# Kernel optimization log

Measured on AMD Instinct MI355X. Metric: run time of the kernel, lower is better.

The kernel has to match this reference:

```python
import jax, jax.numpy as jnp
import numpy as np

B, C, H, W = 4, 128, 64, 64
HEADS, DH, MEM = 4, 32, 16
HID = HEADS * DH  # 128


def setup_inputs() -> dict:
    key = jax.random.key(0)
    k1, k2, k3, k4, k5 = jax.random.split(key, 5)
    return {
        "x": jax.random.normal(k1, (B, C, H, W), jnp.float32),
        "memory": jax.random.normal(k2, (1, C, 1, MEM), jnp.float32),
        "w_qkv": jax.random.normal(k3, (3 * HID, C), jnp.float32) * 0.05,  # conv1x1, bias=False
        "w_out": jax.random.normal(k4, (C, HID), jnp.float32) * 0.05,      # conv1x1 weight
        "b_out": jax.random.normal(k5, (C,), jnp.float32) * 0.01,          # conv1x1 bias
    }


def reference(x, memory, w_qkv, w_out, b_out):
    b, c, h, w = x.shape
    hw = h * w
    scale = DH ** -0.5

    # flatten spatial, append memory tokens along token axis
    x_flat = x.reshape(b, c, hw)                         # (b, c, hw)
    mem = jnp.broadcast_to(memory[:, :, 0, :], (b, c, MEM))
    x_ext = jnp.concatenate([x_flat, mem], axis=2)       # (b, c, n) n = hw + MEM

    # 1x1 conv QKV projection == channel matmul
    qkv = jnp.einsum('oc,bcn->bon', w_qkv, x_ext)        # (b, 3*HID, n)
    q, k, v = jnp.split(qkv, 3, axis=1)                  # each (b, HID, n)

    def to_heads(t):
        return t.reshape(b, HEADS, DH, -1)               # (b, h, d, n)

    q = to_heads(q) * scale
    k = to_heads(k)
    v = to_heads(v)

    sim = jnp.einsum('bhdi,bhdj->bhij', q, k)            # (b, h, n, n)
    attn = jax.nn.softmax(sim, axis=-1)                  # stable softmax (amax-sub inside)
    out = jnp.einsum('bhij,bhdj->bhid', attn, v)         # (b, h, n, d)

    out = out[:, :, :hw]                                 # drop memory-token queries
    out = out.transpose(0, 1, 3, 2).reshape(b, HID, h, w)  # b (h d) x y

    return jnp.einsum('oc,bchw->bohw', w_out, out) + b_out[None, :, None, None]
```

## Files before the change

kernel.cpp:

```cpp
#include <hip/hip_runtime.h>
#include <hip/hip_bf16.h>

constexpr int NQ   = 4096;
constexpr int NKV  = 4112;
constexpr int NP   = 4160;
constexpr int CDIM = 128;
constexpr int NSL  = 4;
constexpr float QSC = 0.17677669529663687f * 1.4426950408889634f;

typedef __attribute__((ext_vector_type(8)))  short bf16x8;
typedef __attribute__((ext_vector_type(4)))  short bf16x4;
typedef __attribute__((ext_vector_type(4)))  unsigned short u16x4;
typedef __attribute__((ext_vector_type(4)))  float f32x4;
typedef __attribute__((ext_vector_type(16))) float f32x16;

static __device__ __forceinline__ unsigned short bfbits(float f) {
  __hip_bfloat16 h = __float2bfloat16(f);
  return *reinterpret_cast<unsigned short*>(&h);
}
static __device__ __forceinline__ unsigned pk2(float a, float b) {
  return (unsigned)bfbits(a) | ((unsigned)bfbits(b) << 16);
}
static __device__ __forceinline__ float b2f(unsigned short u) {
  unsigned x = (unsigned)u << 16;
  return *reinterpret_cast<float*>(&x);
}

__global__ __launch_bounds__(256) void k1_qkv(
    const float* __restrict__ x, const float* __restrict__ memry,
    const float* __restrict__ wqkv, const float* __restrict__ wout,
    __hip_bfloat16* __restrict__ Qt, __hip_bfloat16* __restrict__ Kt,
    __hip_bfloat16* __restrict__ Vt, __hip_bfloat16* __restrict__ Wb) {
  __shared__ __align__(16) __hip_bfloat16 xt[64][136];
  const int b  = blockIdx.y;
  const int zz = blockIdx.z;
  const int nb = blockIdx.x * 64;
  const int t  = threadIdx.x;
  const int wv = t >> 6, ln = t & 63;

  if (blockIdx.x == 0 && b == 0 && zz == 0) {
    for (int i = t; i < CDIM * CDIM; i += 256) Wb[i] = __float2bfloat16(wout[i]);
  }

  {
    const int n = nb + ln;
    #pragma unroll
    for (int i = 0; i < 16; ++i) {
      const int c = wv * 32 + 2 * i;
      float v0 = 0.f, v1 = 0.f;
      if (n < NQ)        { v0 = x[((size_t)b * CDIM + c) * NQ + n];
                           v1 = x[((size_t)b * CDIM + c + 1) * NQ + n]; }
      else if (n < NKV)  { v0 = memry[c * 16 + (n - NQ)];
                           v1 = memry[(c + 1) * 16 + (n - NQ)]; }
      *reinterpret_cast<unsigned*>(&xt[ln][c]) =
          (unsigned)bfbits(v0) | ((unsigned)bfbits(v1) << 16);
    }
  }
  __syncthreads();

  const int li = ln & 15, g = ln >> 4;
  bf16x8 xa[4][4];
  #pragma unroll
  for (int nt = 0; nt < 4; ++nt)
    #pragma unroll
    for (int k = 0; k < 4; ++k)
      xa[nt][k] = *reinterpret_cast<const bf16x8*>(&xt[nt * 16 + li][k * 32 + 8 * g]);

  #pragma unroll
  for (int oi = 0; oi < 3; ++oi) {
    const int ot = zz * 12 + wv * 3 + oi;
    bf16x8 wf[4];
    #pragma unroll
    for (int k = 0; k < 4; ++k) {
      const float* wp = &wqkv[(size_t)(ot * 16 + li) * CDIM + k * 32 + 8 * g];
      const float4 f0 = *reinterpret_cast<const float4*>(wp);
      const float4 f1 = *reinterpret_cast<const float4*>(wp + 4);
      bf16x8 wc;
      wc[0] = (short)bfbits(f0.x); wc[1] = (short)bfbits(f0.y);
      wc[2] = (short)bfbits(f0.z); wc[3] = (short)bfbits(f0.w);
      wc[4] = (short)bfbits(f1.x); wc[5] = (short)bfbits(f1.y);
      wc[6] = (short)bfbits(f1.z); wc[7] = (short)bfbits(f1.w);
      wf[k] = wc;
    }
    #pragma unroll
    for (int nt = 0; nt < 4; ++nt) {
      f32x4 a; a[0] = a[1] = a[2] = a[3] = 0.f;
      if (ot < 16) {
        #pragma unroll
        for (int k = 0; k < 4; ++k)
          a = __builtin_amdgcn_mfma_f32_16x16x32_bf16(xa[nt][k], wf[k], a, 0, 0, 0);
        const int o = ot * 16 + li;
        const int h = (o >> 5) & 3, d = o & 31;
        if (ot < 8) {
          #pragma unroll
          for (int r = 0; r < 4; ++r) {
            const int n = nb + nt * 16 + 4 * g + r;
            Qt[((size_t)(b * 4 + h) * NP + n) * 32 + d] = __float2bfloat16(a[r] * QSC);
          }
        } else {
          #pragma unroll
          for (int r = 0; r < 4; ++r) {
            const int n = nb + nt * 16 + 4 * g + r;
            Kt[((size_t)(b * 4 + h) * NP + n) * 32 + d] = __float2bfloat16(a[r]);
          }
        }
      } else {
        #pragma unroll
        for (int k = 0; k < 4; ++k)
          a = __builtin_amdgcn_mfma_f32_16x16x32_bf16(wf[k], xa[nt][k], a, 0, 0, 0);
        #pragma unroll
        for (int r = 0; r < 4; ++r) {
          const int o = ot * 16 + 4 * g + r;
          const int h = (o >> 5) & 3, d = o & 31;
          const int n = nb + nt * 16 + li;
          Vt[((size_t)(b * 4 + h) * 32 + d) * NP + n] = __float2bfloat16(a[r]);
        }
      }
    }
  }
}


#if __has_builtin(__builtin_amdgcn_mfma_f32_32x32x8bf16_1k)
#define HAS_PV8 1
#else
#define HAS_PV8 0
#endif

#if HAS_PV8
__device__ __forceinline__ void half32(
    const bf16x8& kf0, const bf16x8& kf1,
    const bf16x4& vf0, const bf16x4& vf1, const bf16x4& vf2, const bf16x4& vf3,
    const bf16x8& q0, const bf16x8& q1, const f32x16& z,
    f32x16& acc, float& l0, float& l1, float& l2, float& l3) {
  __builtin_amdgcn_s_setprio(1);
  f32x16 s = __builtin_amdgcn_mfma_f32_32x32x16_bf16(kf0, q0, z, 0, 0, 0);
  s = __builtin_amdgcn_mfma_f32_32x32x16_bf16(kf1, q1, s, 0, 0, 0);
  __builtin_amdgcn_s_setprio(0);
  float p[16];
  #pragma unroll
  for (int r = 0; r < 16; ++r) p[r] = __builtin_amdgcn_exp2f(s[r]);
  l0 += (p[0] + p[1]) + (p[2] + p[3]);
  l1 += (p[4] + p[5]) + (p[6] + p[7]);
  l2 += (p[8] + p[9]) + (p[10] + p[11]);
  l3 += (p[12] + p[13]) + (p[14] + p[15]);
  union UU { unsigned u[2]; bf16x4 v; };
  UU a0, a1, a2, a3;
  a0.u[0] = pk2(p[0], p[1]);   a0.u[1] = pk2(p[2], p[3]);
  a1.u[0] = pk2(p[4], p[5]);   a1.u[1] = pk2(p[6], p[7]);
  a2.u[0] = pk2(p[8], p[9]);   a2.u[1] = pk2(p[10], p[11]);
  a3.u[0] = pk2(p[12], p[13]); a3.u[1] = pk2(p[14], p[15]);
  __builtin_amdgcn_s_setprio(1);
  acc = __builtin_amdgcn_mfma_f32_32x32x8bf16_1k(a0.v, vf0, acc, 0, 0, 0);
  acc = __builtin_amdgcn_mfma_f32_32x32x8bf16_1k(a1.v, vf1, acc, 0, 0, 0);
  acc = __builtin_amdgcn_mfma_f32_32x32x8bf16_1k(a2.v, vf2, acc, 0, 0, 0);
  acc = __builtin_amdgcn_mfma_f32_32x32x8bf16_1k(a3.v, vf3, acc, 0, 0, 0);
  __builtin_amdgcn_s_setprio(0);
}
#else
__device__ __forceinline__ void half32_fb(
    const bf16x8& kf0, const bf16x8& kf1,
    const bf16x8& vh0, const bf16x8& vh1, int hi,
    const bf16x8& q0, const bf16x8& q1, const f32x16& z,
    f32x16& acc, float& l0, float& l1, float& l2, float& l3) {
  f32x16 s = __builtin_amdgcn_mfma_f32_32x32x16_bf16(kf0, q0, z, 0, 0, 0);
  s = __builtin_amdgcn_mfma_f32_32x32x16_bf16(kf1, q1, s, 0, 0, 0);
  float p[16];
  #pragma unroll
  for (int r = 0; r < 16; ++r) p[r] = __builtin_amdgcn_exp2f(s[r]);
  l0 += (p[0] + p[1]) + (p[2] + p[3]);
  l1 += (p[4] + p[5]) + (p[6] + p[7]);
  l2 += (p[8] + p[9]) + (p[10] + p[11]);
  l3 += (p[12] + p[13]) + (p[14] + p[15]);
  unsigned a0u0 = pk2(p[0], p[1]),   a0u1 = pk2(p[2], p[3]);
  unsigned a1u0 = pk2(p[4], p[5]),   a1u1 = pk2(p[6], p[7]);
  unsigned a2u0 = pk2(p[8], p[9]),   a2u1 = pk2(p[10], p[11]);
  unsigned a3u0 = pk2(p[12], p[13]), a3u1 = pk2(p[14], p[15]);
  union U8 { unsigned u[4]; bf16x8 v; };
  {
    const unsigned s0 = __shfl_xor(hi ? a0u0 : a1u0, 32, 64);
    const unsigned s1 = __shfl_xor(hi ? a0u1 : a1u1, 32, 64);
    U8 f;
    f.u[0] = hi ? s0 : a0u0; f.u[1] = hi ? s1 : a0u1;
    f.u[2] = hi ? a1u0 : s0; f.u[3] = hi ? a1u1 : s1;
    acc = __builtin_amdgcn_mfma_f32_32x32x16_bf16(f.v, vh0, acc, 0, 0, 0);
  }
  {
    const unsigned s0 = __shfl_xor(hi ? a2u0 : a3u0, 32, 64);
    const unsigned s1 = __shfl_xor(hi ? a2u1 : a3u1, 32, 64);
    U8 f;
    f.u[0] = hi ? s0 : a2u0; f.u[1] = hi ? s1 : a2u1;
    f.u[2] = hi ? a3u0 : s0; f.u[3] = hi ? a3u1 : s1;
    acc = __builtin_amdgcn_mfma_f32_32x32x16_bf16(f.v, vh1, acc, 0, 0, 0);
  }
}
#endif

__global__ __launch_bounds__(256, 3) void k2_attn(
    const __hip_bfloat16* __restrict__ Qt, const __hip_bfloat16* __restrict__ Kt,
    const __hip_bfloat16* __restrict__ Vt, __hip_bfloat16* __restrict__ Pb,
    float* __restrict__ Lb) {
  __shared__ __align__(16) unsigned char smem[16384];

  const int wg  = blockIdx.x;
  const int xcd = wg & 7;
  const int i   = wg >> 3;
  const int bh  = 2 * xcd + (i & 1);
  const int sl  = (i >> 1) & 3;
  const int iq  = i >> 3;
  const int wv  = threadIdx.x >> 6, lane = threadIdx.x & 63;
  const int lq  = lane & 31, hi = lane >> 5;
  const int qbase = iq * 256 + wv * 64;

  const bf16x8 qA0 = *reinterpret_cast<const bf16x8*>(
      Qt + ((size_t)bh * NP + qbase + lq) * 32 + 8 * hi);
  const bf16x8 qA1 = *reinterpret_cast<const bf16x8*>(
      Qt + ((size_t)bh * NP + qbase + lq) * 32 + 16 + 8 * hi);
  const bf16x8 qB0 = *reinterpret_cast<const bf16x8*>(
      Qt + ((size_t)bh * NP + qbase + 32 + lq) * 32 + 8 * hi);
  const bf16x8 qB1 = *reinterpret_cast<const bf16x8*>(
      Qt + ((size_t)bh * NP + qbase + 32 + lq) * 32 + 16 + 8 * hi);

  const int kb0 = sl * 1024;
  const __hip_bfloat16* Ksrc = Kt + ((size_t)bh * NP + kb0 + (wv >> 1) * 32 + lq) * 32
                                  + (wv & 1) * 16 + 8 * hi;
  const __hip_bfloat16* Vsrc = Vt + ((size_t)bh * 32 + lq) * NP + kb0 + wv * 16 + 8 * hi;
  const int kdst = wv * 1024 + lane * 16;
  const int vdst = (wv >> 1) * 2048 + ((wv & 1) * 2 + hi) * 512 + lq * 8;
  const int rdv  = hi * 256 + lq * 8;

  f32x16 accA, accB, z;
  #pragma unroll
  for (int q = 0; q < 16; ++q) { accA[q] = 0.f; accB[q] = 0.f; z[q] = 0.f; }
  float la0 = 0.f, la1 = 0.f, la2 = 0.f, la3 = 0.f;
  float lb0 = 0.f, lb1 = 0.f, lb2 = 0.f, lb3 = 0.f;

  bf16x8 kreg = *reinterpret_cast<const bf16x8*>(Ksrc);
  bf16x8 vreg = *reinterpret_cast<const bf16x8*>(Vsrc);

#define WRITE_KV(basep)                                                        \
  {                                                                            \
    *reinterpret_cast<bf16x8*>((basep) + kdst) = kreg;                         \
    bf16x4 vlo, vhi;                                                           \
    vlo[0] = vreg[0]; vlo[1] = vreg[1]; vlo[2] = vreg[2]; vlo[3] = vreg[3];    \
    vhi[0] = vreg[4]; vhi[1] = vreg[5]; vhi[2] = vreg[6]; vhi[3] = vreg[7];    \
    *reinterpret_cast<bf16x4*>((basep) + 4096 + vdst)       = vlo;             \
    *reinterpret_cast<bf16x4*>((basep) + 4096 + vdst + 256) = vhi;             \
  }

  WRITE_KV(smem)
  kreg = *reinterpret_cast<const bf16x8*>(Ksrc + 2048);
  vreg = *reinterpret_cast<const bf16x8*>(Vsrc + 64);

  for (int t = 0; t < 16; ++t) {
    __syncthreads();
    const int p = t & 1;
    if (t < 15) {
      unsigned char* nbuf = smem + (p ^ 1) * 8192;
      WRITE_KV(nbuf)
      if (t < 14) {
        kreg = *reinterpret_cast<const bf16x8*>(Ksrc + (size_t)(t + 2) * 2048);
        vreg = *reinterpret_cast<const bf16x8*>(Vsrc + (t + 2) * 64);
      }
    }
    const unsigned char* kbuf = smem + p * 8192;
    const unsigned char* vbase = kbuf + 4096;

    #pragma unroll
    for (int st = 0; st < 2; ++st) {
      const bf16x8 kf0 = *reinterpret_cast<const bf16x8*>(kbuf + st * 2048 + lane * 16);
      const bf16x8 kf1 = *reinterpret_cast<const bf16x8*>(kbuf + st * 2048 + 1024 + lane * 16);
#if HAS_PV8
      const unsigned char* vb = vbase + st * 2048;
      const bf16x4 vf0 = *reinterpret_cast<const bf16x4*>(vb + rdv);
      const bf16x4 vf1 = *reinterpret_cast<const bf16x4*>(vb + 512 + rdv);
      const bf16x4 vf2 = *reinterpret_cast<const bf16x4*>(vb + 1024 + rdv);
      const bf16x4 vf3 = *reinterpret_cast<const bf16x4*>(vb + 1536 + rdv);
      half32(kf0, kf1, vf0, vf1, vf2, vf3, qA0, qA1, z, accA, la0, la1, la2, la3);
      half32(kf0, kf1, vf0, vf1, vf2, vf3, qB0, qB1, z, accB, lb0, lb1, lb2, lb3);
#else
      const unsigned char* vb = vbase + st * 2048;
      union { bf16x4 h[2]; bf16x8 w; } vh0, vh1;
      vh0.h[0] = *reinterpret_cast<const bf16x4*>(vb + hi * 512 + lq * 8);
      vh0.h[1] = *reinterpret_cast<const bf16x4*>(vb + hi * 512 + 256 + lq * 8);
      vh1.h[0] = *reinterpret_cast<const bf16x4*>(vb + (2 + hi) * 512 + lq * 8);
      vh1.h[1] = *reinterpret_cast<const bf16x4*>(vb + (2 + hi) * 512 + 256 + lq * 8);
      half32_fb(kf0, kf1, vh0.w, vh1.w, hi, qA0, qA1, z, accA, la0, la1, la2, la3);
      half32_fb(kf0, kf1, vh0.w, vh1.w, hi, qB0, qB1, z, accB, lb0, lb1, lb2, lb3);
#endif
    }
  }
#undef WRITE_KV

  if (sl == NSL - 1) {
    const __hip_bfloat16* Kp   = Kt + (size_t)bh * NP * 32 + (size_t)lq * 32 + 8 * hi;
    const __hip_bfloat16* Vrow = Vt + ((size_t)bh * 32 + lq) * NP;
    const int kb = 4096;
    const bf16x8 kf0 = *reinterpret_cast<const bf16x8*>(Kp + (size_t)kb * 32);
    const bf16x8 kf1 = *reinterpret_cast<const bf16x8*>(Kp + (size_t)kb * 32 + 16);
#if HAS_PV8
    const bf16x4 vt0 = *reinterpret_cast<const bf16x4*>(Vrow + kb + 4 * hi);
    const bf16x4 vt1 = *reinterpret_cast<const bf16x4*>(Vrow + kb + 8 + 4 * hi);
#else
    const bf16x8 vt8 = *reinterpret_cast<const bf16x8*>(Vrow + kb + 8 * hi);
#endif
    #pragma unroll
    for (int hf = 0; hf < 2; ++hf) {
      const bf16x8 q0 = hf ? qB0 : qA0;
      const bf16x8 q1 = hf ? qB1 : qA1;
      f32x16 s = __builtin_amdgcn_mfma_f32_32x32x16_bf16(kf0, q0, z, 0, 0, 0);
      s = __builtin_amdgcn_mfma_f32_32x32x16_bf16(kf1, q1, s, 0, 0, 0);
      float p_[8];
      #pragma unroll
      for (int r = 0; r < 8; ++r) p_[r] = __builtin_amdgcn_exp2f(s[r]);
      const float s01 = (p_[0] + p_[1]) + (p_[2] + p_[3]);
      const float s23 = (p_[4] + p_[5]) + (p_[6] + p_[7]);
      if (hf) { lb0 += s01; lb1 += s23; } else { la0 += s01; la1 += s23; }
#if HAS_PV8
      union UU { unsigned u[2]; bf16x4 v; };
      UU a0, a1;
      a0.u[0] = pk2(p_[0], p_[1]); a0.u[1] = pk2(p_[2], p_[3]);
      a1.u[0] = pk2(p_[4], p_[5]); a1.u[1] = pk2(p_[6], p_[7]);
      if (hf) {
        accB = __builtin_amdgcn_mfma_f32_32x32x8bf16_1k(a0.v, vt0, accB, 0, 0, 0);
        accB = __builtin_amdgcn_mfma_f32_32x32x8bf16_1k(a1.v, vt1, accB, 0, 0, 0);
      } else {
        accA = __builtin_amdgcn_mfma_f32_32x32x8bf16_1k(a0.v, vt0, accA, 0, 0, 0);
        accA = __builtin_amdgcn_mfma_f32_32x32x8bf16_1k(a1.v, vt1, accA, 0, 0, 0);
      }
#else
      unsigned a0u0 = pk2(p_[0], p_[1]), a0u1 = pk2(p_[2], p_[3]);
      unsigned a1u0 = pk2(p_[4], p_[5]), a1u1 = pk2(p_[6], p_[7]);
      union U8 { unsigned u[4]; bf16x8 v; };
      const unsigned s0 = __shfl_xor(hi ? a0u0 : a1u0, 32, 64);
      const unsigned s1 = __shfl_xor(hi ? a0u1 : a1u1, 32, 64);
      U8 f;
      f.u[0] = hi ? s0 : a0u0; f.u[1] = hi ? s1 : a0u1;
      f.u[2] = hi ? a1u0 : s0; f.u[3] = hi ? a1u1 : s1;
      if (hf) accB = __builtin_amdgcn_mfma_f32_32x32x16_bf16(f.v, vt8, accB, 0, 0, 0);
      else    accA = __builtin_amdgcn_mfma_f32_32x32x16_bf16(f.v, vt8, accA, 0, 0, 0);
#endif
    }
  }

  __hip_bfloat16* PpA = Pb + (((size_t)sl * 16 + bh) * NQ + qbase) * 32;
  #pragma unroll
  for (int r = 0; r < 16; ++r) {
    const int q = (r & 3) + 8 * (r >> 2) + 4 * hi;
    PpA[(size_t)q * 32 + lq] = __float2bfloat16(accA[r]);
    PpA[(size_t)(q + 32) * 32 + lq] = __float2bfloat16(accB[r]);
  }
  float lsA = (la0 + la1) + (la2 + la3);
  float lsB = (lb0 + lb1) + (lb2 + lb3);
  lsA += __shfl_xor(lsA, 32, 64);
  lsB += __shfl_xor(lsB, 32, 64);
  if (hi == 0) {
    Lb[((size_t)sl * 16 + bh) * NQ + qbase + lq] = lsA;
    Lb[((size_t)sl * 16 + bh) * NQ + qbase + 32 + lq] = lsB;
  }
}

__global__ __launch_bounds__(256) void k2b_combine(
    const __hip_bfloat16* __restrict__ Pb, const float* __restrict__ Lb,
    __hip_bfloat16* __restrict__ att) {
  constexpr size_t PS = (size_t)16 * NQ * 32;
  constexpr size_t LS = (size_t)16 * NQ;
  const int wg  = blockIdx.x;
  const int xcd = wg & 7;
  const int i   = wg >> 3;
  const int bh  = 2 * xcd + (i & 1);
  const int j   = i >> 1;
  const int u   = j * 256 + threadIdx.x;
  const int q   = u >> 3;
  const int d0  = (u & 7) * 4;
  const size_t qi = (size_t)bh * NQ + q;

  float l = 0.f;
  #pragma unroll
  for (int s = 0; s < NSL; ++s) l += Lb[s * LS + qi];
  const float inv = 1.f / l;

  float4 o = make_float4(0.f, 0.f, 0.f, 0.f);
  #pragma unroll
  for (int s = 0; s < NSL; ++s) {
    const u16x4 f = *reinterpret_cast<const u16x4*>(Pb + s * PS + qi * 32 + d0);
    o.x += b2f(f[0]); o.y += b2f(f[1]); o.z += b2f(f[2]); o.w += b2f(f[3]);
  }
  *reinterpret_cast<uint2*>(att + qi * 32 + d0) =
      make_uint2(pk2(o.x * inv, o.y * inv), pk2(o.z * inv, o.w * inv));
}

__global__ __launch_bounds__(256) void k3_proj(
    const __hip_bfloat16* __restrict__ att, const __hip_bfloat16* __restrict__ Wb,
    const float* __restrict__ bout, float* __restrict__ out) {
  const int b = blockIdx.y, nb = blockIdx.x * 32;
  const int wv = threadIdx.x >> 6, lane = threadIdx.x & 63;
  const int li = lane & 15, g = lane >> 4;

  bf16x8 wf[2][4];
  float bo[2][4];
  #pragma unroll
  for (int tt = 0; tt < 2; ++tt) {
    const int ot = 2 * wv + tt;
    #pragma unroll
    for (int k = 0; k < 4; ++k)
      wf[tt][k] = *reinterpret_cast<const bf16x8*>(
          &Wb[(size_t)(ot * 16 + li) * CDIM + k * 32 + 8 * g]);
    #pragma unroll
    for (int r = 0; r < 4; ++r) bo[tt][r] = bout[ot * 16 + 4 * g + r];
  }
  #pragma unroll
  for (int nt = 0; nt < 2; ++nt) {
    bf16x8 bfr[4];
    #pragma unroll
    for (int k = 0; k < 4; ++k)
      bfr[k] = *reinterpret_cast<const bf16x8*>(
          &att[(((size_t)(b * 4 + k)) * NQ + nb + nt * 16 + li) * 32 + 8 * g]);
    #pragma unroll
    for (int tt = 0; tt < 2; ++tt) {
      f32x4 a; a[0] = a[1] = a[2] = a[3] = 0.f;
      #pragma unroll
      for (int k = 0; k < 4; ++k)
        a = __builtin_amdgcn_mfma_f32_16x16x32_bf16(wf[tt][k], bfr[k], a, 0, 0, 0);
      const int ot = 2 * wv + tt;
      #pragma unroll
      for (int r = 0; r < 4; ++r)
        out[((size_t)b * CDIM + ot * 16 + 4 * g + r) * NQ + nb + nt * 16 + li] =
            a[r] + bo[tt][r];
    }
  }
}

extern "C" void kernel_launch(void* const* d_in, const int* in_sizes, int n_in,
                              void* d_out, int out_size, void* d_ws, size_t ws_size,
                              hipStream_t stream) {
  const float* x    = (const float*)d_in[0];
  const float* memp = (const float*)d_in[1];
  const float* wqkv = (const float*)d_in[2];
  const float* wout = (const float*)d_in[3];
  const float* bout = (const float*)d_in[4];
  float* out = (float*)d_out;

  char* ws = (char*)d_ws;
  const size_t SZ  = (size_t)16 * NP * 32 * 2;
  const size_t PSZ = (size_t)NSL * 16 * NQ * 32 * 2;
  const size_t LSZ = (size_t)NSL * 16 * NQ * 4;
  const size_t ASZ = (size_t)16 * NQ * 32 * 2;
  __hip_bfloat16* Qt  = (__hip_bfloat16*)(ws);
  __hip_bfloat16* Kt  = (__hip_bfloat16*)(ws + SZ);
  __hip_bfloat16* Vt  = (__hip_bfloat16*)(ws + 2 * SZ);
  __hip_bfloat16* Pbf = (__hip_bfloat16*)(ws + 3 * SZ);
  float*          Lbf = (float*)(ws + 3 * SZ + PSZ);
  __hip_bfloat16* att = (__hip_bfloat16*)(ws + 3 * SZ + PSZ + LSZ);
  __hip_bfloat16* Wb  = (__hip_bfloat16*)(ws + 3 * SZ + PSZ + LSZ + ASZ);

  hipLaunchKernelGGL(k1_qkv, dim3(65, 4, 2), dim3(256), 0, stream,
                     x, memp, wqkv, wout, Qt, Kt, Vt, Wb);
  hipLaunchKernelGGL(k2_attn, dim3(1024), dim3(256), 0, stream,
                     Qt, Kt, Vt, Pbf, Lbf);
  hipLaunchKernelGGL(k2b_combine, dim3(2048), dim3(256), 0, stream, Pbf, Lbf, att);
  hipLaunchKernelGGL(k3_proj, dim3(128, 4), dim3(256), 0, stream, att, Wb, bout, out);
}
```

Baseline: 95.39 us.

## Pre-tile V layout and stream K/V into LDS with direct global-to-LDS loads

The QKV kernel now writes V in a tiled layout that already matches the attention kernel's LDS arrangement. This lets the attention loop use global_load_lds to copy K and V straight into shared memory, with no register staging and no repacking. The setprio hints around the MFMAs are also removed. Risks: the loop now prefetches on every iteration, including one tile past the end at t=15, which may read past the slice. Correctness also depends on the wait and barrier semantics of the async LDS loads.

```diff
diff --git a/kernel.cpp b/kernel.cpp
--- a/kernel.cpp
+++ b/kernel.cpp
@@ -6,6 +6,7 @@
 constexpr int NP   = 4160;
 constexpr int CDIM = 128;
 constexpr int NSL  = 4;
+constexpr int VTILE = 2048;
 constexpr float QSC = 0.17677669529663687f * 1.4426950408889634f;
 
 typedef __attribute__((ext_vector_type(8)))  short bf16x8;
@@ -25,6 +26,11 @@
   unsigned x = (unsigned)u << 16;
   return *reinterpret_cast<float*>(&x);
 }
+
+#define GLOAD_LDS16(gsrc, ldst)                                               \
+  __builtin_amdgcn_global_load_lds(                                           \
+      (const __attribute__((address_space(1))) unsigned int*)(gsrc),          \
+      (__attribute__((address_space(3))) unsigned int*)(ldst), 16, 0, 0)
 
 __global__ __launch_bounds__(256) void k1_qkv(
     const float* __restrict__ x, const float* __restrict__ memry,
@@ -108,12 +114,15 @@
         #pragma unroll
         for (int k = 0; k < 4; ++k)
           a = __builtin_amdgcn_mfma_f32_16x16x32_bf16(wf[k], xa[nt][k], a, 0, 0, 0);
+        const int n = nb + nt * 16 + li;
+        const size_t vb = (size_t)(b * 4) * 65 * VTILE
+                        + (size_t)(n >> 6) * VTILE + ((n >> 5) & 1) * 1024
+                        + ((n >> 3) & 3) * 256 + ((n >> 2) & 1) * 128 + (n & 3);
         #pragma unroll
         for (int r = 0; r < 4; ++r) {
           const int o = ot * 16 + 4 * g + r;
           const int h = (o >> 5) & 3, d = o & 31;
-          const int n = nb + nt * 16 + li;
-          Vt[((size_t)(b * 4 + h) * 32 + d) * NP + n] = __float2bfloat16(a[r]);
+          Vt[vb + (size_t)h * 65 * VTILE + d * 4] = __float2bfloat16(a[r]);
         }
       }
     }
@@ -133,10 +142,8 @@
     const bf16x4& vf0, const bf16x4& vf1, const bf16x4& vf2, const bf16x4& vf3,
     const bf16x8& q0, const bf16x8& q1, const f32x16& z,
     f32x16& acc, float& l0, float& l1, float& l2, float& l3) {
-  __builtin_amdgcn_s_setprio(1);
   f32x16 s = __builtin_amdgcn_mfma_f32_32x32x16_bf16(kf0, q0, z, 0, 0, 0);
   s = __builtin_amdgcn_mfma_f32_32x32x16_bf16(kf1, q1, s, 0, 0, 0);
-  __builtin_amdgcn_s_setprio(0);
   float p[16];
   #pragma unroll
   for (int r = 0; r < 16; ++r) p[r] = __builtin_amdgcn_exp2f(s[r]);
@@ -150,12 +157,10 @@
   a1.u[0] = pk2(p[4], p[5]);   a1.u[1] = pk2(p[6], p[7]);
   a2.u[0] = pk2(p[8], p[9]);   a2.u[1] = pk2(p[10], p[11]);
   a3.u[0] = pk2(p[12], p[13]); a3.u[1] = pk2(p[14], p[15]);
-  __builtin_amdgcn_s_setprio(1);
   acc = __builtin_amdgcn_mfma_f32_32x32x8bf16_1k(a0.v, vf0, acc, 0, 0, 0);
   acc = __builtin_amdgcn_mfma_f32_32x32x8bf16_1k(a1.v, vf1, acc, 0, 0, 0);
   acc = __builtin_amdgcn_mfma_f32_32x32x8bf16_1k(a2.v, vf2, acc, 0, 0, 0);
   acc = __builtin_amdgcn_mfma_f32_32x32x8bf16_1k(a3.v, vf3, acc, 0, 0, 0);
-  __builtin_amdgcn_s_setprio(0);
 }
 #else
 __device__ __forceinline__ void half32_fb(
@@ -224,9 +229,9 @@
   const int kb0 = sl * 1024;
   const __hip_bfloat16* Ksrc = Kt + ((size_t)bh * NP + kb0 + (wv >> 1) * 32 + lq) * 32
                                   + (wv & 1) * 16 + 8 * hi;
-  const __hip_bfloat16* Vsrc = Vt + ((size_t)bh * 32 + lq) * NP + kb0 + wv * 16 + 8 * hi;
-  const int kdst = wv * 1024 + lane * 16;
-  const int vdst = (wv >> 1) * 2048 + ((wv & 1) * 2 + hi) * 512 + lq * 8;
+  const __hip_bfloat16* Vsrc = Vt + (size_t)bh * 65 * VTILE
+                                  + (size_t)(kb0 >> 6) * VTILE + threadIdx.x * 8;
+  const int kofs = wv * 1024;
   const int rdv  = hi * 256 + lq * 8;
 
   f32x16 accA, accB, z;
@@ -235,33 +240,16 @@
   float la0 = 0.f, la1 = 0.f, la2 = 0.f, la3 = 0.f;
   float lb0 = 0.f, lb1 = 0.f, lb2 = 0.f, lb3 = 0.f;
 
-  bf16x8 kreg = *reinterpret_cast<const bf16x8*>(Ksrc);
-  bf16x8 vreg = *reinterpret_cast<const bf16x8*>(Vsrc);
-
-#define WRITE_KV(basep)                                                        \
-  {                                                                            \
-    *reinterpret_cast<bf16x8*>((basep) + kdst) = kreg;                         \
-    bf16x4 vlo, vhi;                                                           \
-    vlo[0] = vreg[0]; vlo[1] = vreg[1]; vlo[2] = vreg[2]; vlo[3] = vreg[3];    \
-    vhi[0] = vreg[4]; vhi[1] = vreg[5]; vhi[2] = vreg[6]; vhi[3] = vreg[7];    \
-    *reinterpret_cast<bf16x4*>((basep) + 4096 + vdst)       = vlo;             \
-    *reinterpret_cast<bf16x4*>((basep) + 4096 + vdst + 256) = vhi;             \
-  }
-
-  WRITE_KV(smem)
-  kreg = *reinterpret_cast<const bf16x8*>(Ksrc + 2048);
-  vreg = *reinterpret_cast<const bf16x8*>(Vsrc + 64);
+  GLOAD_LDS16(Ksrc, smem + kofs);
+  GLOAD_LDS16(Vsrc, smem + 4096 + kofs);
 
   for (int t = 0; t < 16; ++t) {
     __syncthreads();
     const int p = t & 1;
-    if (t < 15) {
+    {
       unsigned char* nbuf = smem + (p ^ 1) * 8192;
-      WRITE_KV(nbuf)
-      if (t < 14) {
-        kreg = *reinterpret_cast<const bf16x8*>(Ksrc + (size_t)(t + 2) * 2048);
-        vreg = *reinterpret_cast<const bf16x8*>(Vsrc + (t + 2) * 64);
-      }
+      GLOAD_LDS16(Ksrc + (size_t)(t + 1) * 2048, nbuf + kofs);
+      GLOAD_LDS16(Vsrc + (size_t)(t + 1) * 2048, nbuf + 4096 + kofs);
     }
     const unsigned char* kbuf = smem + p * 8192;
     const unsigned char* vbase = kbuf + 4096;
@@ -290,19 +278,21 @@
 #endif
     }
   }
-#undef WRITE_KV
 
   if (sl == NSL - 1) {
-    const __hip_bfloat16* Kp   = Kt + (size_t)bh * NP * 32 + (size_t)lq * 32 + 8 * hi;
-    const __hip_bfloat16* Vrow = Vt + ((size_t)bh * 32 + lq) * NP;
+    const __hip_bfloat16* Kp = Kt + (size_t)bh * NP * 32 + (size_t)lq * 32 + 8 * hi;
+    const __hip_bfloat16* Vtt = Vt + (size_t)bh * 65 * VTILE + (size_t)64 * VTILE;
     const int kb = 4096;
     const bf16x8 kf0 = *reinterpret_cast<const bf16x8*>(Kp + (size_t)kb * 32);
     const bf16x8 kf1 = *reinterpret_cast<const bf16x8*>(Kp + (size_t)kb * 32 + 16);
 #if HAS_PV8
-    const bf16x4 vt0 = *reinterpret_cast<const bf16x4*>(Vrow + kb + 4 * hi);
-    const bf16x4 vt1 = *reinterpret_cast<const bf16x4*>(Vrow + kb + 8 + 4 * hi);
+    const bf16x4 vt0 = *reinterpret_cast<const bf16x4*>(Vtt + hi * 128 + lq * 4);
+    const bf16x4 vt1 = *reinterpret_cast<const bf16x4*>(Vtt + 256 + hi * 128 + lq * 4);
 #else
-    const bf16x8 vt8 = *reinterpret_cast<const bf16x8*>(Vrow + kb + 8 * hi);
+    union { bf16x4 h[2]; bf16x8 w; } vt8u;
+    vt8u.h[0] = *reinterpret_cast<const bf16x4*>(Vtt + hi * 256 + lq * 4 + 0);
+    vt8u.h[1] = *reinterpret_cast<const bf16x4*>(Vtt + hi * 256 + lq * 4 + 128);
+    const bf16x8 vt8 = vt8u.w;
 #endif
     #pragma unroll
     for (int hf = 0; hf < 2; ++hf) {
@@ -443,16 +433,17 @@
 
   char* ws = (char*)d_ws;
   const size_t SZ  = (size_t)16 * NP * 32 * 2;
+  const size_t VSZ = (size_t)16 * 65 * VTILE * 2;
   const size_t PSZ = (size_t)NSL * 16 * NQ * 32 * 2;
   const size_t LSZ = (size_t)NSL * 16 * NQ * 4;
   const size_t ASZ = (size_t)16 * NQ * 32 * 2;
   __hip_bfloat16* Qt  = (__hip_bfloat16*)(ws);
   __hip_bfloat16* Kt  = (__hip_bfloat16*)(ws + SZ);
   __hip_bfloat16* Vt  = (__hip_bfloat16*)(ws + 2 * SZ);
-  __hip_bfloat16* Pbf = (__hip_bfloat16*)(ws + 3 * SZ);
-  float*          Lbf = (float*)(ws + 3 * SZ + PSZ);
-  __hip_bfloat16* att = (__hip_bfloat16*)(ws + 3 * SZ + PSZ + LSZ);
-  __hip_bfloat16* Wb  = (__hip_bfloat16*)(ws + 3 * SZ + PSZ + LSZ + ASZ);
+  __hip_bfloat16* Pbf = (__hip_bfloat16*)(ws + 2 * SZ + VSZ);
+  float*          Lbf = (float*)(ws + 2 * SZ + VSZ + PSZ);
+  __hip_bfloat16* att = (__hip_bfloat16*)(ws + 2 * SZ + VSZ + PSZ + LSZ);
+  __hip_bfloat16* Wb  = (__hip_bfloat16*)(ws + 2 * SZ + VSZ + PSZ + LSZ + ASZ);
 
   hipLaunchKernelGGL(k1_qkv, dim3(65, 4, 2), dim3(256), 0, stream,
                      x, memp, wqkv, wout, Qt, Kt, Vt, Wb);
```

New measurement: 89.23 us. 1.07x faster.
